# Performance work log

Hardware: AMD Instinct MI355X
Metric: run time of the kernel (lower is better)

## Reference

```python
import jax, jax.numpy as jnp
import numpy as np

ITEMS_TOTAL = 50000
DIM = 64
BATCH = 16
N_PER_GRAPH = 50


def setup_inputs() -> dict:
    key = jax.random.key(0)
    k1, k2, k3, k4 = jax.random.split(key, 4)
    nodes = jax.random.randint(k1, (BATCH * N_PER_GRAPH,), 0, ITEMS_TOTAL, dtype=jnp.int64)
    nodes_output = jax.random.normal(k2, (BATCH * N_PER_GRAPH, DIM), dtype=jnp.float32)
    emb_table = jax.random.normal(k3, (ITEMS_TOTAL, DIM), dtype=jnp.float32)
    alpha = jax.random.uniform(k4, (ITEMS_TOTAL, 1), dtype=jnp.float32)  # torch.rand init
    return {"nodes": nodes, "nodes_output": nodes_output, "emb_table": emb_table,
            "alpha": alpha, "n_per_graph": N_PER_GRAPH}


def reference(nodes, nodes_output, emb_table, alpha, n_per_graph):
    items_total, dim = emb_table.shape
    n = int(n_per_graph)
    b = nodes.shape[0] // n
    idx_b = nodes.reshape(b, n)            # (B, n) item indices per graph
    feat_b = nodes_output.reshape(b, n, dim)  # (B, n, F)

    def per_graph(idx, feat):
        # beta: 1 for items present in this graph, 0 otherwise
        beta = jnp.zeros((items_total, 1), dtype=emb_table.dtype).at[idx].set(1.0)
        # gate the full table: untouched rows keep emb, touched rows scaled by (1-alpha)
        embed = (1.0 - beta * alpha) * emb_table          # (items_total, F)
        updated = embed[idx] + alpha[idx] * feat          # (n, F)
        return embed.at[idx].set(updated)

    return jax.vmap(per_graph)(idx_b, feat_b)             # (B, items_total, F)
```

## Files before the change

kernel.cpp:

```cpp
#include <hip/hip_runtime.h>
#include <hip/hip_bf16.h>


#define DIM 64
#define SEGS (DIM / 4)
#define BLOCK 256
#define ROWS_PER_BLOCK 512

__global__ __launch_bounds__(BLOCK) void ggu_kernel(
    const int* __restrict__ nodes,
    const float4* __restrict__ feat,
    const float4* __restrict__ emb,
    const float* __restrict__ alpha,
    float4* __restrict__ out,
    int items, int n, int blocks_per_graph)
{
    const int b     = blockIdx.x / blocks_per_graph;
    const int chunk = blockIdx.x % blocks_per_graph;
    const int row0  = chunk * ROWS_PER_BLOCK;

    extern __shared__ unsigned int smem[];
    const int nwords = (items + 31) >> 5;
    unsigned int* bitmap = smem;
    int* sidx = (int*)(smem + nwords);

    for (int w = threadIdx.x; w < nwords; w += BLOCK) bitmap[w] = 0u;
    __syncthreads();
    for (int j = threadIdx.x; j < n; j += BLOCK) {
        int id = nodes[b * n + j];
        sidx[j] = id;
        atomicOr(&bitmap[id >> 5], 1u << (id & 31));
    }
    __syncthreads();

    const int seg  = threadIdx.x & (SEGS - 1);
    const int rloc = threadIdx.x >> 4;
    const int rows_per_iter = BLOCK >> 4;
    const int rend = min(row0 + ROWS_PER_BLOCK, items);

    const size_t out_base = (size_t)b * items * SEGS;

    for (int r = row0 + rloc; r < rend; r += rows_per_iter) {
        float4 e = emb[(size_t)r * SEGS + seg];
        unsigned int w = bitmap[r >> 5];
        if (w & (1u << (r & 31))) {
            int jlast = -1;
            #pragma unroll 1
            for (int j = 0; j < n; ++j)
                if (sidx[j] == r) jlast = j;
            float a = alpha[r];
            float4 f = feat[(size_t)(b * n + jlast) * SEGS + seg];
            float om = 1.0f - a;
            e.x = om * e.x + a * f.x;
            e.y = om * e.y + a * f.y;
            e.z = om * e.z + a * f.z;
            e.w = om * e.w + a * f.w;
        }
        out[out_base + (size_t)r * SEGS + seg] = e;
    }
}

extern "C" void kernel_launch(void* const* d_in, const int* in_sizes, int n_in,
                              void* d_out, int out_size, void* d_ws, size_t ws_size,
                              hipStream_t stream) {
    const int*   nodes = (const int*)d_in[0];
    const float* feat  = (const float*)d_in[1];
    const float* emb   = (const float*)d_in[2];
    const float* alpha = (const float*)d_in[3];

    const int items = in_sizes[3];
    const int B     = out_size / (items * DIM);
    const int total_nodes = in_sizes[0];
    const int n     = total_nodes / B;

    const int blocks_per_graph = (items + ROWS_PER_BLOCK - 1) / ROWS_PER_BLOCK;
    const int grid = B * blocks_per_graph;

    const int nwords = (items + 31) >> 5;
    const size_t lds_bytes = (size_t)(nwords + n) * sizeof(unsigned int);

    ggu_kernel<<<grid, BLOCK, lds_bytes, stream>>>(
        nodes, (const float4*)feat, (const float4*)emb, alpha,
        (float4*)d_out, items, n, blocks_per_graph);
}
```

Measured before the change: 243.6 us.

## Tile by item rows across all graphs, reusing each embedding load for every batch

The grid now covers only item-row chunks of 32 rows. Each block loads an embedding row once and writes it to all B graph outputs, instead of reloading the row per graph. Per-block per-row graph masks built from all node indices replace the full-table per-graph bitmap, and stores are nontemporal. Every block now scans all B*n node indices, and the per-graph mask is limited to 32 graphs, so larger batches would break.

```diff
diff --git a/kernel.cpp b/kernel.cpp
--- a/kernel.cpp
+++ b/kernel.cpp
@@ -5,58 +5,80 @@
 #define DIM 64
 #define SEGS (DIM / 4)
 #define BLOCK 256
-#define ROWS_PER_BLOCK 512
+#define RPB 32
 
+typedef float v4f __attribute__((ext_vector_type(4)));
+
+__device__ __forceinline__ void nt_store(float4* p, const float4& v) {
+    __builtin_nontemporal_store(*(const v4f*)&v, (v4f*)p);
+}
+
+template <int CB>
 __global__ __launch_bounds__(BLOCK) void ggu_kernel(
     const int* __restrict__ nodes,
     const float4* __restrict__ feat,
     const float4* __restrict__ emb,
     const float* __restrict__ alpha,
     float4* __restrict__ out,
-    int items, int n, int blocks_per_graph)
+    int items, int n, int Brt)
 {
-    const int b     = blockIdx.x / blocks_per_graph;
-    const int chunk = blockIdx.x % blocks_per_graph;
-    const int row0  = chunk * ROWS_PER_BLOCK;
+    const int B = (CB > 0) ? CB : Brt;
+    const int row0 = blockIdx.x * RPB;
 
     extern __shared__ unsigned int smem[];
-    const int nwords = (items + 31) >> 5;
-    unsigned int* bitmap = smem;
-    int* sidx = (int*)(smem + nwords);
+    unsigned int* rowmask = smem;
+    int* sidx = (int*)(smem + RPB);
 
-    for (int w = threadIdx.x; w < nwords; w += BLOCK) bitmap[w] = 0u;
+    const int total = B * n;
+    if (threadIdx.x < RPB) rowmask[threadIdx.x] = 0u;
     __syncthreads();
-    for (int j = threadIdx.x; j < n; j += BLOCK) {
-        int id = nodes[b * n + j];
-        sidx[j] = id;
-        atomicOr(&bitmap[id >> 5], 1u << (id & 31));
+    for (int t = threadIdx.x; t < total; t += BLOCK) {
+        int id = nodes[t];
+        sidx[t] = id;
+        int local = id - row0;
+        if ((unsigned)local < (unsigned)RPB)
+            atomicOr(&rowmask[local], 1u << (t / n));
     }
     __syncthreads();
 
     const int seg  = threadIdx.x & (SEGS - 1);
     const int rloc = threadIdx.x >> 4;
-    const int rows_per_iter = BLOCK >> 4;
-    const int rend = min(row0 + ROWS_PER_BLOCK, items);
+    const int rend = min(row0 + RPB, items);
+    const size_t bstride = (size_t)items * SEGS;
 
-    const size_t out_base = (size_t)b * items * SEGS;
+    for (int r = row0 + rloc; r < rend; r += (BLOCK / SEGS)) {
+        const float4 e = emb[(size_t)r * SEGS + seg];
+        const unsigned int mask = rowmask[r - row0];
+        float4* po = out + (size_t)r * SEGS + seg;
 
-    for (int r = row0 + rloc; r < rend; r += rows_per_iter) {
-        float4 e = emb[(size_t)r * SEGS + seg];
-        unsigned int w = bitmap[r >> 5];
-        if (w & (1u << (r & 31))) {
-            int jlast = -1;
-            #pragma unroll 1
-            for (int j = 0; j < n; ++j)
-                if (sidx[j] == r) jlast = j;
-            float a = alpha[r];
-            float4 f = feat[(size_t)(b * n + jlast) * SEGS + seg];
-            float om = 1.0f - a;
-            e.x = om * e.x + a * f.x;
-            e.y = om * e.y + a * f.y;
-            e.z = om * e.z + a * f.z;
-            e.w = om * e.w + a * f.w;
+        if (mask == 0u) {
+            #pragma unroll
+            for (int b = 0; b < ((CB > 0) ? CB : 1); ++b) {
+                if (CB > 0) { nt_store(po, e); po += bstride; }
+            }
+            if (CB == 0) {
+                for (int b = 0; b < B; ++b) { nt_store(po, e); po += bstride; }
+            }
+        } else {
+            const float a  = alpha[r];
+            const float om = 1.0f - a;
+            for (int b = 0; b < B; ++b) {
+                float4 v = e;
+                if ((mask >> b) & 1u) {
+                    int jlast = 0;
+                    #pragma unroll 1
+                    for (int j = 0; j < n; ++j)
+                        if (sidx[b * n + j] == r) jlast = j;
+                    const float4 f = feat[(size_t)(b * n + jlast) * SEGS + seg];
+                    v.x = om * e.x + a * f.x;
+                    v.y = om * e.y + a * f.y;
+                    v.z = om * e.z + a * f.z;
+                    v.w = om * e.w + a * f.w;
+                }
+                nt_store(po, v);
+                po += bstride;
+            }
         }
-        out[out_base + (size_t)r * SEGS + seg] = e;
     }
 }
 
@@ -70,16 +92,18 @@
 
     const int items = in_sizes[3];
     const int B     = out_size / (items * DIM);
-    const int total_nodes = in_sizes[0];
-    const int n     = total_nodes / B;
+    const int n     = in_sizes[0] / B;
 
-    const int blocks_per_graph = (items + ROWS_PER_BLOCK - 1) / ROWS_PER_BLOCK;
-    const int grid = B * blocks_per_graph;
+    const int grid = (items + RPB - 1) / RPB;
+    const size_t lds_bytes = (size_t)(RPB + B * n) * sizeof(unsigned int);
 
-    const int nwords = (items + 31) >> 5;
-    const size_t lds_bytes = (size_t)(nwords + n) * sizeof(unsigned int);
-
-    ggu_kernel<<<grid, BLOCK, lds_bytes, stream>>>(
-        nodes, (const float4*)feat, (const float4*)emb, alpha,
-        (float4*)d_out, items, n, blocks_per_graph);
+    if (B == 16) {
+        ggu_kernel<16><<<grid, BLOCK, lds_bytes, stream>>>(
+            nodes, (const float4*)feat, (const float4*)emb, alpha,
+            (float4*)d_out, items, n, B);
+    } else {
+        ggu_kernel<0><<<grid, BLOCK, lds_bytes, stream>>>(
+            nodes, (const float4*)feat, (const float4*)emb, alpha,
+            (float4*)d_out, items, n, B);
+    }
 }
```

New measurement: 233.3 us. 1.04x faster.
